# Performance work log

Hardware: AMD Instinct MI355X
Metric: run time of the kernel (lower is better)

The kernel has to match this reference:

```python
import jax, jax.numpy as jnp
import numpy as np

NUM_HEADS = 16
EPS = 1e-6


def setup_inputs() -> dict:
    key = jax.random.key(0)
    ks = jax.random.split(key, 5)
    L, N, E = 2048, 8, 1024
    scale = 1.0 / np.sqrt(E)
    return {
        "query": jax.random.normal(ks[0], (L, N, E), jnp.float32),
        "Wq": jax.random.normal(ks[1], (E, E), jnp.float32) * scale,
        "Wk": jax.random.normal(ks[2], (E, E), jnp.float32) * scale,
        "Wv": jax.random.normal(ks[3], (E, E), jnp.float32) * scale,
        "Wo": jax.random.normal(ks[4], (E, E), jnp.float32) * scale,
    }


def reference(query, Wq, Wk, Wv, Wo):
    # cosFormer non-causal linear attention (self.causal = False branch).
    L, N, E = query.shape
    h = NUM_HEADS
    d = E // h

    # projections (nn.Linear, no bias) + ReLU feature map on q, k
    q = jax.nn.relu(query @ Wq.T)
    k = jax.nn.relu(query @ Wk.T)  # key defaults to query
    v = query @ Wv.T               # value defaults to query

    # (L, N, E) -> (n = N*h, L, d)
    def split_heads(x):
        return x.reshape(L, N * h, d).transpose(1, 0, 2)

    q, k, v = split_heads(q), split_heads(k), split_heads(v)

    # cos/sin reweighting: index = pi/2 * arange(1..m) / m, m = L (src==tgt)
    idx = (jnp.pi / 2) * jnp.arange(1, L + 1, dtype=jnp.float32) / L
    sin = jnp.sin(idx)[None, :, None]  # (1, L, 1)
    cos = jnp.cos(idx)[None, :, None]
    q_ = jnp.concatenate([q * sin, q * cos], axis=-1)  # (n, L, 2d)
    k_ = jnp.concatenate([k * sin, k * cos], axis=-1)

    # linear attention aggregation: kv_ is only (n, 2d, d)
    kv = jnp.einsum('nld,nlm->ndm', k_, v)
    z = 1.0 / jnp.maximum(jnp.einsum('nld,nd->nl', q_, k_.sum(axis=1)), EPS)
    attn = jnp.einsum('nld,ndm->nlm', q_, kv) * z[..., None]  # (n, L, d)

    # (n, L, d) -> (L, N, E), then output projection
    attn = attn.transpose(1, 0, 2).reshape(L, N, E)
    return attn @ Wo.T
```

## Files before the change

### kernel.cpp

```cpp
#include <hip/hip_runtime.h>
#include <math.h>

#define L_DIM 2048
#define N_DIM 8
#define E_DIM 1024
#define H_DIM 16
#define D_DIM 64
#define M_DIM (L_DIM * N_DIM)
#define NHEADS (N_DIM * H_DIM)
#define TWO_D 128
#define K_DIM 1024
#define CH 4
#define LCH (L_DIM / CH)

#define KV_ELEMS (NHEADS * TWO_D * D_DIM)
#define KS_ELEMS (NHEADS * TWO_D)
#define CSTRIDE (KV_ELEMS + KS_ELEMS)

typedef __attribute__((ext_vector_type(8))) __bf16 bf16x8;
typedef __attribute__((ext_vector_type(4))) float f32x4;

__device__ __forceinline__ ushort f2bf(float x) {
    union { float f; unsigned u; } a; a.f = x;
    unsigned r = a.u + 0x7fffu + ((a.u >> 16) & 1u);
    return (ushort)(r >> 16);
}
__device__ __forceinline__ float bf2f(ushort h) {
    union { unsigned u; float f; } a; a.u = ((unsigned)h) << 16;
    return a.f;
}

__device__ __forceinline__ void gload_lds16(const void* g, void* l) {
    __builtin_amdgcn_global_load_lds((const __attribute__((address_space(1))) void*)g,
                                     (__attribute__((address_space(3))) void*)l, 16, 0, 0);
}

__global__ __launch_bounds__(256) void split_fp32(const float* __restrict__ in,
                                                  ushort* __restrict__ hi,
                                                  ushort* __restrict__ lo, int n4) {
    int i = blockIdx.x * 256 + threadIdx.x;
    const int stride = gridDim.x * 256;
    for (; i < n4; i += stride) {
        float4 v = ((const float4*)in)[i];
        ushort h0 = f2bf(v.x), h1 = f2bf(v.y), h2 = f2bf(v.z), h3 = f2bf(v.w);
        ushort l0 = f2bf(v.x - bf2f(h0)), l1 = f2bf(v.y - bf2f(h1));
        ushort l2 = f2bf(v.z - bf2f(h2)), l3 = f2bf(v.w - bf2f(h3));
        ((ushort4*)hi)[i] = make_ushort4(h0, h1, h2, h3);
        ((ushort4*)lo)[i] = make_ushort4(l0, l1, l2, l3);
    }
}

__global__ __launch_bounds__(256) void split_w4(const float* __restrict__ w0,
                                                const float* __restrict__ w1,
                                                const float* __restrict__ w2,
                                                const float* __restrict__ w3,
                                                ushort* __restrict__ hi,
                                                ushort* __restrict__ lo) {
    const int midx = blockIdx.y;
    const float* src = (midx == 0) ? w0 : (midx == 1) ? w1 : (midx == 2) ? w2 : w3;
    hi += (size_t)midx * E_DIM * E_DIM;
    lo += (size_t)midx * E_DIM * E_DIM;
    const int n4 = E_DIM * E_DIM / 4;
    int i = blockIdx.x * 256 + threadIdx.x;
    const int stride = gridDim.x * 256;
    for (; i < n4; i += stride) {
        float4 v = ((const float4*)src)[i];
        ushort h0 = f2bf(v.x), h1 = f2bf(v.y), h2 = f2bf(v.z), h3 = f2bf(v.w);
        ushort l0 = f2bf(v.x - bf2f(h0)), l1 = f2bf(v.y - bf2f(h1));
        ushort l2 = f2bf(v.z - bf2f(h2)), l3 = f2bf(v.w - bf2f(h3));
        ((ushort4*)hi)[i] = make_ushort4(h0, h1, h2, h3);
        ((ushort4*)lo)[i] = make_ushort4(l0, l1, l2, l3);
    }
}

template <int OUTMODE, int NBS>
__global__ __launch_bounds__(512) void gemm3(const ushort* __restrict__ Ahi,
                                             const ushort* __restrict__ Alo,
                                             const ushort* __restrict__ Bhi,
                                             const ushort* __restrict__ Blo,
                                             float* __restrict__ C,
                                             float* __restrict__ C2) {
    __shared__ ushort smem[3][24576];

    const int t = threadIdx.x;
    const int wid = t >> 6;
    const int lane = t & 63;

    const int x = blockIdx.x;
    const int cxcd = x & 7;
    const int j = x >> 3;
    const int mb = cxcd * 16 + j / NBS;
    const int nb = j % NBS;
    const int m0 = mb * 128, n0 = nb * 256;

    const int srow = t >> 2;
    const int sch = t & 3;
    const int gch = sch ^ ((srow >> 1) & 3);
    const ushort* sAh = Ahi + (size_t)(m0 + srow) * K_DIM + gch * 8;
    const ushort* sAl = Alo + (size_t)(m0 + srow) * K_DIM + gch * 8;
    const ushort* sBh = Bhi + (size_t)(n0 + srow) * K_DIM + gch * 8;
    const ushort* sBl = Blo + (size_t)(n0 + srow) * K_DIM + gch * 8;
    const size_t B2 = (size_t)128 * K_DIM;

#define STAGE3(b, kt2)                                                   \
    do {                                                                 \
        const size_t kc_ = (size_t)(kt2) * 32;                           \
        gload_lds16(sAh + kc_, &smem[b][0] + wid * 512);                 \
        gload_lds16(sAl + kc_, &smem[b][4096] + wid * 512);              \
        gload_lds16(sBh + kc_, &smem[b][8192] + wid * 512);              \
        gload_lds16(sBh + B2 + kc_, &smem[b][12288] + wid * 512);        \
        gload_lds16(sBl + kc_, &smem[b][16384] + wid * 512);             \
        gload_lds16(sBl + B2 + kc_, &smem[b][20480] + wid * 512);        \
    } while (0)

    const int wm = wid >> 2;
    const int wn = wid & 3;
    const int lr = lane & 15;
    const int kc = lane >> 4;
    int aoff[4], boff[4];
#pragma unroll
    for (int m = 0; m < 4; ++m) {
        const int r = wm * 64 + m * 16 + lr;
        aoff[m] = r * 32 + ((kc ^ ((r >> 1) & 3)) << 3);
    }
#pragma unroll
    for (int n = 0; n < 4; ++n) {
        const int r = wn * 64 + n * 16 + lr;
        boff[n] = r * 32 + ((kc ^ ((r >> 1) & 3)) << 3);
    }

    f32x4 acc[4][4];
    const f32x4 zv = {0.f, 0.f, 0.f, 0.f};
#pragma unroll
    for (int m = 0; m < 4; ++m)
#pragma unroll
        for (int n = 0; n < 4; ++n) acc[m][n] = zv;

    const int NK = K_DIM / 32;

    STAGE3(0, 0);
    STAGE3(1, 1);
    asm volatile("s_waitcnt vmcnt(6)" ::: "memory");
    __builtin_amdgcn_s_barrier();
    asm volatile("" ::: "memory");

#pragma unroll 1
    for (int kt = 0; kt < NK; ++kt) {
        const int cur = kt % 3;
        if (kt + 2 < NK) STAGE3((kt + 2) % 3, kt + 2);

        const ushort* bb = smem[cur];
        bf16x8 bh[4], bl[4];
#pragma unroll
        for (int n = 0; n < 4; ++n) {
            bh[n] = *(const bf16x8*)&bb[8192 + boff[n]];
            bl[n] = *(const bf16x8*)&bb[16384 + boff[n]];
        }
#pragma unroll
        for (int m = 0; m < 4; ++m) {
            const bf16x8 ah = *(const bf16x8*)&bb[aoff[m]];
            const bf16x8 al = *(const bf16x8*)&bb[4096 + aoff[m]];
            __builtin_amdgcn_s_setprio(1);
#pragma unroll
            for (int n = 0; n < 4; ++n) {
                acc[m][n] = __builtin_amdgcn_mfma_f32_16x16x32_bf16(ah, bh[n], acc[m][n], 0, 0, 0);
                acc[m][n] = __builtin_amdgcn_mfma_f32_16x16x32_bf16(ah, bl[n], acc[m][n], 0, 0, 0);
                acc[m][n] = __builtin_amdgcn_mfma_f32_16x16x32_bf16(al, bh[n], acc[m][n], 0, 0, 0);
            }
            __builtin_amdgcn_s_setprio(0);
        }

        if (kt < NK - 1) {
            if (kt + 2 < NK) {
                asm volatile("s_waitcnt vmcnt(6)" ::: "memory");
            } else {
                asm volatile("s_waitcnt vmcnt(0)" ::: "memory");
            }
            __builtin_amdgcn_s_barrier();
            asm volatile("" ::: "memory");
        }
    }

    const int erow = (lane >> 4) * 4;
    const int ecol = lane & 15;
#pragma unroll
    for (int m = 0; m < 4; ++m) {
        const int grb = m0 + wm * 64 + m * 16 + erow;
#pragma unroll
        for (int n = 0; n < 4; ++n) {
            const int gc = n0 + wn * 64 + n * 16 + ecol;
            f32x4 v = acc[m][n];
#pragma unroll
            for (int q = 0; q < 4; ++q) {
                const int gr = grb + q;
                float val = v[q];
                if constexpr (OUTMODE == 0) {
                    C[(size_t)gr * E_DIM + gc] = val;
                } else if constexpr (OUTMODE == 1) {
                    val = fmaxf(val, 0.f);
                    const int hh = gc >> 6, d = gc & 63;
                    C[((size_t)((gr & 7) * 16 + hh) * L_DIM + (gr >> 3)) * D_DIM + d] = val;
                } else {
                    const int mat = gc >> 10;
                    const int col = gc & 1023;
                    if (mat == 0) val = fmaxf(val, 0.f);
                    const int hh = col >> 6, d = col & 63;
                    float* dst = mat ? C2 : C;
                    dst[((size_t)((gr & 7) * 16 + hh) * L_DIM + (gr >> 3)) * D_DIM + d] = val;
                }
            }
        }
    }
#undef STAGE3
}

__global__ __launch_bounds__(256) void kv_partial(const float* __restrict__ Kh,
                                                  const float* __restrict__ Vh,
                                                  float* __restrict__ kvp) {
    const int g = blockIdx.x;
    const int c = blockIdx.y;
    const int t = threadIdx.x;

    __shared__ float Kt[32][64];
    __shared__ float Vt[32][64];
    __shared__ float sT[32], cT[32];

    const int gi = t >> 3;
    const int gj = t & 7;
    const int i0 = gi * 2, j0 = gj * 8;

    float S[2][8], Cc[2][8];
#pragma unroll
    for (int i = 0; i < 2; ++i)
#pragma unroll
        for (int jj = 0; jj < 8; ++jj) { S[i][jj] = 0.f; Cc[i][jj] = 0.f; }
    float sk[2] = {0.f, 0.f}, ck[2] = {0.f, 0.f};

    for (int lt = 0; lt < LCH; lt += 32) {
        const int lbase = c * LCH + lt;
        const float4* ks = (const float4*)&Kh[((size_t)g * L_DIM + lbase) * D_DIM];
        const float4* vs = (const float4*)&Vh[((size_t)g * L_DIM + lbase) * D_DIM];
        ((float4*)&Kt[0][0])[t] = ks[t];
        ((float4*)&Kt[0][0])[t + 256] = ks[t + 256];
        ((float4*)&Vt[0][0])[t] = vs[t];
        ((float4*)&Vt[0][0])[t + 256] = vs[t + 256];
        if (t < 32) {
            const float ang = 1.57079632679489662f * (float)(lbase + t + 1) / (float)L_DIM;
            sT[t] = sinf(ang);
            cT[t] = cosf(ang);
        }
        __syncthreads();
#pragma unroll 4
        for (int lr = 0; lr < 32; ++lr) {
            const float sl = sT[lr], cl = cT[lr];
            const float k0v = Kt[lr][i0], k1v = Kt[lr][i0 + 1];
            const float ks0 = k0v * sl, ks1 = k1v * sl;
            const float kc0 = k0v * cl, kc1 = k1v * cl;
            sk[0] += ks0; sk[1] += ks1; ck[0] += kc0; ck[1] += kc1;
            float v8[8];
            *(float4*)&v8[0] = *(float4*)&Vt[lr][j0];
            *(float4*)&v8[4] = *(float4*)&Vt[lr][j0 + 4];
#pragma unroll
            for (int jj = 0; jj < 8; ++jj) {
                S[0][jj] = fmaf(ks0, v8[jj], S[0][jj]);
                S[1][jj] = fmaf(ks1, v8[jj], S[1][jj]);
                Cc[0][jj] = fmaf(kc0, v8[jj], Cc[0][jj]);
                Cc[1][jj] = fmaf(kc1, v8[jj], Cc[1][jj]);
            }
        }
        __syncthreads();
    }

    float* kvb = kvp + (size_t)c * CSTRIDE + (size_t)g * TWO_D * D_DIM;
#pragma unroll
    for (int ii = 0; ii < 2; ++ii) {
        *(float4*)&kvb[(size_t)(i0 + ii) * D_DIM + j0] =
            make_float4(S[ii][0], S[ii][1], S[ii][2], S[ii][3]);
        *(float4*)&kvb[(size_t)(i0 + ii) * D_DIM + j0 + 4] =
            make_float4(S[ii][4], S[ii][5], S[ii][6], S[ii][7]);
        *(float4*)&kvb[(size_t)(64 + i0 + ii) * D_DIM + j0] =
            make_float4(Cc[ii][0], Cc[ii][1], Cc[ii][2], Cc[ii][3]);
        *(float4*)&kvb[(size_t)(64 + i0 + ii) * D_DIM + j0 + 4] =
            make_float4(Cc[ii][4], Cc[ii][5], Cc[ii][6], Cc[ii][7]);
    }
    if (gj == 0) {
        float* ksb = kvp + (size_t)c * CSTRIDE + KV_ELEMS + (size_t)g * TWO_D;
        ksb[i0] = sk[0];
        ksb[i0 + 1] = sk[1];
        ksb[64 + i0] = ck[0];
        ksb[64 + i0 + 1] = ck[1];
    }
}

__global__ __launch_bounds__(256) void attn_kernel(const float* __restrict__ Qh,
                                                   const float* __restrict__ kvp,
                                                   ushort* __restrict__ attnHi,
                                                   ushort* __restrict__ attnLo) {
    const int g = blockIdx.x;
    const int lt = blockIdx.y;
    const int nb = g >> 4, hh = g & 15;
    const int t = threadIdx.x;

    __shared__ float kvs[TWO_D][64];
    __shared__ float qT[TWO_D][64];
    __shared__ float sTab[64], cTab[64], ksS[TWO_D], pz[64][4], zs[64];

    {
        const float4* kv4 = (const float4*)(kvp + (size_t)g * TWO_D * D_DIM);
        const size_t cs4 = CSTRIDE / 4;
        float4* kvs4 = (float4*)&kvs[0][0];
        for (int s = t; s < TWO_D * D_DIM / 4; s += 256) {
            float4 a = kv4[s], b = kv4[s + cs4], c = kv4[s + 2 * cs4], d = kv4[s + 3 * cs4];
            kvs4[s] = make_float4(a.x + b.x + c.x + d.x, a.y + b.y + c.y + d.y,
                                  a.z + b.z + c.z + d.z, a.w + b.w + c.w + d.w);
        }
    }
    if (t < TWO_D) {
        const size_t o = KV_ELEMS + (size_t)g * TWO_D + t;
        ksS[t] = kvp[o] + kvp[o + CSTRIDE] + kvp[o + 2 * (size_t)CSTRIDE] + kvp[o + 3 * (size_t)CSTRIDE];
    }

    const int lbase = lt * 64;
    if (t < 64) {
        const float ang = 1.57079632679489662f * (float)(lbase + t + 1) / (float)L_DIM;
        sTab[t] = sinf(ang);
        cTab[t] = cosf(ang);
    }

    const int lq = t >> 2;
    const int dq = (t & 3) * 16;
    float qv[16];
    {
        const float* qrow = Qh + ((size_t)g * L_DIM + lbase + lq) * D_DIM + dq;
        *(float4*)&qv[0] = *(const float4*)&qrow[0];
        *(float4*)&qv[4] = *(const float4*)&qrow[4];
        *(float4*)&qv[8] = *(const float4*)&qrow[8];
        *(float4*)&qv[12] = *(const float4*)&qrow[12];
    }
    __syncthreads();

    {
        const float sl = sTab[lq], cl = cTab[lq];
#pragma unroll
        for (int jj = 0; jj < 16; ++jj) {
            qT[dq + jj][lq] = qv[jj] * sl;
            qT[64 + dq + jj][lq] = qv[jj] * cl;
        }
    }
    __syncthreads();

    {
        const int lz = t >> 2, qz = t & 3;
        float p = 0.f;
#pragma unroll
        for (int i = 0; i < 32; ++i) p = fmaf(qT[qz * 32 + i][lz], ksS[qz * 32 + i], p);
        pz[lz][qz] = p;
    }
    __syncthreads();
    if (t < 64) {
        const float s = pz[t][0] + pz[t][1] + pz[t][2] + pz[t][3];
        zs[t] = 1.0f / fmaxf(s, 1e-6f);
    }
    __syncthreads();

    const int ml = (t >> 4) * 4;
    const int nd = (t & 15) * 4;
    float acc[4][4];
#pragma unroll
    for (int i = 0; i < 4; ++i)
#pragma unroll
        for (int jj = 0; jj < 4; ++jj) acc[i][jj] = 0.f;

    for (int i = 0; i < TWO_D; ++i) {
        float4 a = *(float4*)&qT[i][ml];
        float4 b = *(float4*)&kvs[i][nd];
        acc[0][0] = fmaf(a.x, b.x, acc[0][0]); acc[0][1] = fmaf(a.x, b.y, acc[0][1]);
        acc[0][2] = fmaf(a.x, b.z, acc[0][2]); acc[0][3] = fmaf(a.x, b.w, acc[0][3]);
        acc[1][0] = fmaf(a.y, b.x, acc[1][0]); acc[1][1] = fmaf(a.y, b.y, acc[1][1]);
        acc[1][2] = fmaf(a.y, b.z, acc[1][2]); acc[1][3] = fmaf(a.y, b.w, acc[1][3]);
        acc[2][0] = fmaf(a.z, b.x, acc[2][0]); acc[2][1] = fmaf(a.z, b.y, acc[2][1]);
        acc[2][2] = fmaf(a.z, b.z, acc[2][2]); acc[2][3] = fmaf(a.z, b.w, acc[2][3]);
        acc[3][0] = fmaf(a.w, b.x, acc[3][0]); acc[3][1] = fmaf(a.w, b.y, acc[3][1]);
        acc[3][2] = fmaf(a.w, b.z, acc[3][2]); acc[3][3] = fmaf(a.w, b.w, acc[3][3]);
    }

#pragma unroll
    for (int r = 0; r < 4; ++r) {
        const float z = zs[ml + r];
        const float o0 = acc[r][0] * z, o1 = acc[r][1] * z;
        const float o2 = acc[r][2] * z, o3 = acc[r][3] * z;
        ushort4 hv, lv;
        hv.x = f2bf(o0); lv.x = f2bf(o0 - bf2f(hv.x));
        hv.y = f2bf(o1); lv.y = f2bf(o1 - bf2f(hv.y));
        hv.z = f2bf(o2); lv.z = f2bf(o2 - bf2f(hv.z));
        hv.w = f2bf(o3); lv.w = f2bf(o3 - bf2f(hv.w));
        const size_t base = (size_t)((lbase + ml + r) * N_DIM + nb) * E_DIM + hh * 64 + nd;
        *(ushort4*)&attnHi[base] = hv;
        *(ushort4*)&attnLo[base] = lv;
    }
}

extern "C" void kernel_launch(void* const* d_in, const int* in_sizes, int n_in,
                              void* d_out, int out_size, void* d_ws, size_t ws_size,
                              hipStream_t stream) {
    const float* X = (const float*)d_in[0];
    const float* Wq = (const float*)d_in[1];
    const float* Wk = (const float*)d_in[2];
    const float* Wv = (const float*)d_in[3];
    const float* Wo = (const float*)d_in[4];
    float* out = (float*)d_out;

    char* ws = (char*)d_ws;
    ushort* Xhi = (ushort*)(ws + 0);
    ushort* Xlo = (ushort*)(ws + 33554432);
    ushort* Whi = (ushort*)(ws + 67108864);
    ushort* Wlo = (ushort*)(ws + 75497472);
    float* kvp  = (float*)(ws + 83886080);
    float* bufA = (float*)(ws + 100925440);

    float* Kh = out;
    float* Vh = bufA;
    float* Qh = out;

    const size_t WMAT = (size_t)E_DIM * E_DIM;

    split_fp32<<<2048, 256, 0, stream>>>(X, Xhi, Xlo, M_DIM * E_DIM / 4);
    split_w4<<<dim3(64, 4), 256, 0, stream>>>(Wq, Wk, Wv, Wo, Whi, Wlo);

    gemm3<2, 8><<<1024, 512, 0, stream>>>(Xhi, Xlo, Whi + 1 * WMAT, Wlo + 1 * WMAT, Kh, Vh);

    kv_partial<<<dim3(NHEADS, CH), 256, 0, stream>>>(Kh, Vh, kvp);

    gemm3<1, 4><<<512, 512, 0, stream>>>(Xhi, Xlo, Whi + 0 * WMAT, Wlo + 0 * WMAT, Qh, nullptr);

    attn_kernel<<<dim3(NHEADS, L_DIM / 64), 256, 0, stream>>>(Qh, kvp, Xhi, Xlo);

    gemm3<0, 4><<<512, 512, 0, stream>>>(Xhi, Xlo, Whi + 3 * WMAT, Wlo + 3 * WMAT, out, nullptr);
}
```

Before: 574.6 us.

## Enlarge GEMM tile to 256x256 with double-buffered LDS pipeline

The split-bf16 GEMM tile grows from 128x256 to 256x256, so each wave holds an 8x4 accumulator set and the grid is halved. The LDS pipeline drops from three stages to two, with plain __syncthreads replacing the hand-tuned vmcnt waits and the setprio hints. The larger tile is meant to raise arithmetic intensity and cut global/LDS traffic per FLOP. In exchange it adds register pressure (launch_bounds 512,2) and fewer blocks for the hardware, and the two-stage pipeline with a full barrier hides load latency less well.

```diff
diff --git a/kernel.cpp b/kernel.cpp
--- a/kernel.cpp
+++ b/kernel.cpp
@@ -74,13 +74,13 @@
 }
 
 template <int OUTMODE, int NBS>
-__global__ __launch_bounds__(512) void gemm3(const ushort* __restrict__ Ahi,
-                                             const ushort* __restrict__ Alo,
-                                             const ushort* __restrict__ Bhi,
-                                             const ushort* __restrict__ Blo,
-                                             float* __restrict__ C,
-                                             float* __restrict__ C2) {
-    __shared__ ushort smem[3][24576];
+__global__ __launch_bounds__(512, 2) void gemm2(const ushort* __restrict__ Ahi,
+                                                const ushort* __restrict__ Alo,
+                                                const ushort* __restrict__ Bhi,
+                                                const ushort* __restrict__ Blo,
+                                                float* __restrict__ C,
+                                                float* __restrict__ C2) {
+    __shared__ ushort smem[2][32768];
 
     const int t = threadIdx.x;
     const int wid = t >> 6;
@@ -89,38 +89,39 @@
     const int x = blockIdx.x;
     const int cxcd = x & 7;
     const int j = x >> 3;
-    const int mb = cxcd * 16 + j / NBS;
+    const int mb = cxcd * 8 + j / NBS;
     const int nb = j % NBS;
-    const int m0 = mb * 128, n0 = nb * 256;
+    const int m0 = mb * 256, n0 = nb * 256;
 
     const int srow = t >> 2;
     const int sch = t & 3;
     const int gch = sch ^ ((srow >> 1) & 3);
-    const ushort* sAh = Ahi + (size_t)(m0 + srow) * K_DIM + gch * 8;
-    const ushort* sAl = Alo + (size_t)(m0 + srow) * K_DIM + gch * 8;
-    const ushort* sBh = Bhi + (size_t)(n0 + srow) * K_DIM + gch * 8;
-    const ushort* sBl = Blo + (size_t)(n0 + srow) * K_DIM + gch * 8;
-    const size_t B2 = (size_t)128 * K_DIM;
-
-#define STAGE3(b, kt2)                                                   \
-    do {                                                                 \
-        const size_t kc_ = (size_t)(kt2) * 32;                           \
-        gload_lds16(sAh + kc_, &smem[b][0] + wid * 512);                 \
-        gload_lds16(sAl + kc_, &smem[b][4096] + wid * 512);              \
-        gload_lds16(sBh + kc_, &smem[b][8192] + wid * 512);              \
-        gload_lds16(sBh + B2 + kc_, &smem[b][12288] + wid * 512);        \
-        gload_lds16(sBl + kc_, &smem[b][16384] + wid * 512);             \
-        gload_lds16(sBl + B2 + kc_, &smem[b][20480] + wid * 512);        \
+    const size_t aOff = (size_t)(m0 + srow) * K_DIM + gch * 8;
+    const size_t bOff = (size_t)(n0 + srow) * K_DIM + gch * 8;
+    const size_t H128 = (size_t)128 * K_DIM;
+
+#define STAGE(b, kt1)                                             \
+    do {                                                          \
+        const size_t kc_ = (size_t)(kt1) * 32;                    \
+        ushort* d = (ushort*)&smem[b][0] + wid * 512;             \
+        gload_lds16(Ahi + aOff + kc_, d);                         \
+        gload_lds16(Ahi + aOff + H128 + kc_, d + 4096);           \
+        gload_lds16(Alo + aOff + kc_, d + 8192);                  \
+        gload_lds16(Alo + aOff + H128 + kc_, d + 12288);          \
+        gload_lds16(Bhi + bOff + kc_, d + 16384);                 \
+        gload_lds16(Bhi + bOff + H128 + kc_, d + 20480);          \
+        gload_lds16(Blo + bOff + kc_, d + 24576);                 \
+        gload_lds16(Blo + bOff + H128 + kc_, d + 28672);          \
     } while (0)
 
     const int wm = wid >> 2;
     const int wn = wid & 3;
     const int lr = lane & 15;
     const int kc = lane >> 4;
-    int aoff[4], boff[4];
-#pragma unroll
-    for (int m = 0; m < 4; ++m) {
-        const int r = wm * 64 + m * 16 + lr;
+    int aoff[8], boff[4];
+#pragma unroll
+    for (int m = 0; m < 8; ++m) {
+        const int r = wm * 128 + m * 16 + lr;
         aoff[m] = r * 32 + ((kc ^ ((r >> 1) & 3)) << 3);
     }
 #pragma unroll
@@ -129,63 +130,49 @@
         boff[n] = r * 32 + ((kc ^ ((r >> 1) & 3)) << 3);
     }
 
-    f32x4 acc[4][4];
+    f32x4 acc[8][4];
     const f32x4 zv = {0.f, 0.f, 0.f, 0.f};
 #pragma unroll
-    for (int m = 0; m < 4; ++m)
+    for (int m = 0; m < 8; ++m)
 #pragma unroll
         for (int n = 0; n < 4; ++n) acc[m][n] = zv;
 
     const int NK = K_DIM / 32;
 
-    STAGE3(0, 0);
-    STAGE3(1, 1);
-    asm volatile("s_waitcnt vmcnt(6)" ::: "memory");
-    __builtin_amdgcn_s_barrier();
-    asm volatile("" ::: "memory");
+    STAGE(0, 0);
+    __syncthreads();
 
 #pragma unroll 1
     for (int kt = 0; kt < NK; ++kt) {
-        const int cur = kt % 3;
-        if (kt + 2 < NK) STAGE3((kt + 2) % 3, kt + 2);
-
-        const ushort* bb = smem[cur];
+        const int cb = kt & 1;
+        if (kt + 1 < NK) STAGE(cb ^ 1, kt + 1);
+
+        const ushort* bb = smem[cb];
         bf16x8 bh[4], bl[4];
 #pragma unroll
         for (int n = 0; n < 4; ++n) {
-            bh[n] = *(const bf16x8*)&bb[8192 + boff[n]];
-            bl[n] = *(const bf16x8*)&bb[16384 + boff[n]];
-        }
-#pragma unroll
-        for (int m = 0; m < 4; ++m) {
+            bh[n] = *(const bf16x8*)&bb[16384 + boff[n]];
+            bl[n] = *(const bf16x8*)&bb[24576 + boff[n]];
+        }
+#pragma unroll
+        for (int m = 0; m < 8; ++m) {
             const bf16x8 ah = *(const bf16x8*)&bb[aoff[m]];
-            const bf16x8 al = *(const bf16x8*)&bb[4096 + aoff[m]];
-            __builtin_amdgcn_s_setprio(1);
+            const bf16x8 al = *(const bf16x8*)&bb[8192 + aoff[m]];
 #pragma unroll
             for (int n = 0; n < 4; ++n) {
                 acc[m][n] = __builtin_amdgcn_mfma_f32_16x16x32_bf16(ah, bh[n], acc[m][n], 0, 0, 0);
                 acc[m][n] = __builtin_amdgcn_mfma_f32_16x16x32_bf16(ah, bl[n], acc[m][n], 0, 0, 0);
                 acc[m][n] = __builtin_amdgcn_mfma_f32_16x16x32_bf16(al, bh[n], acc[m][n], 0, 0, 0);
             }
-            __builtin_amdgcn_s_setprio(0);
-        }
-
-        if (kt < NK - 1) {
-            if (kt + 2 < NK) {
-                asm volatile("s_waitcnt vmcnt(6)" ::: "memory");
-            } else {
-                asm volatile("s_waitcnt vmcnt(0)" ::: "memory");
-            }
-            __builtin_amdgcn_s_barrier();
-            asm volatile("" ::: "memory");
-        }
+        }
+        __syncthreads();
     }
 
     const int erow = (lane >> 4) * 4;
     const int ecol = lane & 15;
 #pragma unroll
-    for (int m = 0; m < 4; ++m) {
-        const int grb = m0 + wm * 64 + m * 16 + erow;
+    for (int m = 0; m < 8; ++m) {
+        const int grb = m0 + wm * 128 + m * 16 + erow;
 #pragma unroll
         for (int n = 0; n < 4; ++n) {
             const int gc = n0 + wn * 64 + n * 16 + ecol;
@@ -205,13 +192,13 @@
                     const int col = gc & 1023;
                     if (mat == 0) val = fmaxf(val, 0.f);
                     const int hh = col >> 6, d = col & 63;
-                    float* dst = mat ? C2 : C;
-                    dst[((size_t)((gr & 7) * 16 + hh) * L_DIM + (gr >> 3)) * D_DIM + d] = val;
+                    float* dstc = mat ? C2 : C;
+                    dstc[((size_t)((gr & 7) * 16 + hh) * L_DIM + (gr >> 3)) * D_DIM + d] = val;
                 }
             }
         }
     }
-#undef STAGE3
+#undef STAGE
 }
 
 __global__ __launch_bounds__(256) void kv_partial(const float* __restrict__ Kh,
@@ -427,13 +414,13 @@
     split_fp32<<<2048, 256, 0, stream>>>(X, Xhi, Xlo, M_DIM * E_DIM / 4);
     split_w4<<<dim3(64, 4), 256, 0, stream>>>(Wq, Wk, Wv, Wo, Whi, Wlo);
 
-    gemm3<2, 8><<<1024, 512, 0, stream>>>(Xhi, Xlo, Whi + 1 * WMAT, Wlo + 1 * WMAT, Kh, Vh);
+    gemm2<2, 8><<<512, 512, 0, stream>>>(Xhi, Xlo, Whi + 1 * WMAT, Wlo + 1 * WMAT, Kh, Vh);
 
     kv_partial<<<dim3(NHEADS, CH), 256, 0, stream>>>(Kh, Vh, kvp);
 
-    gemm3<1, 4><<<512, 512, 0, stream>>>(Xhi, Xlo, Whi + 0 * WMAT, Wlo + 0 * WMAT, Qh, nullptr);
+    gemm2<1, 4><<<256, 512, 0, stream>>>(Xhi, Xlo, Whi + 0 * WMAT, Wlo + 0 * WMAT, Qh, nullptr);
 
     attn_kernel<<<dim3(NHEADS, L_DIM / 64), 256, 0, stream>>>(Qh, kvp, Xhi, Xlo);
 
-    gemm3<0, 4><<<512, 512, 0, stream>>>(Xhi, Xlo, Whi + 3 * WMAT, Wlo + 3 * WMAT, out, nullptr);
-}
+    gemm2<0, 4><<<256, 512, 0, stream>>>(Xhi, Xlo, Whi + 3 * WMAT, Wlo + 3 * WMAT, out, nullptr);
+}
```

After: 538.0 us. 6.4% less time.
